# Kernel optimization log

Hardware: AMD Instinct MI355X
Metric: run time of the kernel (lower is better)

The kernel has to match this reference:

```python
import jax, jax.numpy as jnp
import numpy as np

N = 50000   # nodes
E = 800000  # edges
D = 256     # num_features == embedding_num
L = 3       # gcn layers
G = 512     # graphs in batch


def setup_inputs() -> dict:
    key = jax.random.key(0)
    ks = jax.random.split(key, 7)
    x = jax.random.normal(ks[0], (N, D), dtype=jnp.float32)
    edge_index = jax.random.randint(ks[1], (2, E), 0, N, dtype=jnp.int32)
    batch = jnp.sort(jax.random.randint(ks[2], (N,), 0, G, dtype=jnp.int32))
    s = 0.05
    Ws1 = jax.random.normal(ks[3], (L, D, D), dtype=jnp.float32) * s
    bs1 = jnp.zeros((L, D), dtype=jnp.float32)
    Ws2 = jax.random.normal(ks[4], (L, D, D), dtype=jnp.float32) * s
    bs2 = jnp.zeros((L, D), dtype=jnp.float32)
    return {"x": x, "edge_index": edge_index, "batch": batch,
            "Ws1": Ws1, "bs1": bs1, "Ws2": Ws2, "bs2": bs2}


def reference(x, edge_index, batch, Ws1, bs1, Ws2, bs2):
    src, dst = edge_index[0], edge_index[1]
    h = x
    xs = []
    for i in range(L):
        # GINConv (eps=0): h_i' = MLP( h_i + sum_{j->i} h_j )
        agg = h + jax.ops.segment_sum(h[src], dst, num_segments=N)  # [N, D]
        t = jnp.maximum(agg @ Ws1[i] + bs1[i], 0.0)                 # inner ReLU
        h = jnp.maximum(t @ Ws2[i] + bs2[i], 0.0)                   # outer F.relu
        xs.append(h)
    # global mean pool per layer output, keyed by graph id
    ones = jnp.ones((N, 1), dtype=x.dtype)
    counts = jnp.clip(jax.ops.segment_sum(ones, batch, num_segments=G), 1.0)  # [G,1]
    pooled = [jax.ops.segment_sum(h_i, batch, num_segments=G) / counts for h_i in xs]
    graph_embed = jnp.concatenate(pooled, axis=1)  # [G, L*D]
    node_embed = jnp.concatenate(xs, axis=1)       # [N, L*D]
    return graph_embed, node_embed
```

## Files before the change

kernel.cpp:

```cpp
#include <hip/hip_runtime.h>

#define NN 50000
#define EE 800000
#define DD 256
#define LL 3
#define GG 512
#define MPAD 50048

typedef __attribute__((ext_vector_type(4))) _Float16 half4;
typedef __attribute__((ext_vector_type(8))) _Float16 half8;
typedef __attribute__((ext_vector_type(16))) float floatx16;

__global__ void k_convert(const float* __restrict__ x, _Float16* __restrict__ h16) {
    int i = blockIdx.x * 256 + threadIdx.x;
    if (i >= NN * DD / 4) return;
    float4 v = ((const float4*)x)[i];
    half4 o;
    o.x = (_Float16)v.x; o.y = (_Float16)v.y; o.z = (_Float16)v.z; o.w = (_Float16)v.w;
    ((half4*)h16)[i] = o;
}

__global__ void k_hist(const int* __restrict__ dst, int* __restrict__ deg, int e) {
    int i = blockIdx.x * blockDim.x + threadIdx.x;
    if (i < e) atomicAdd(&deg[dst[i]], 1);
}

__global__ void k_scan1(const int* __restrict__ deg, int* __restrict__ rp,
                        int* __restrict__ bsum, int n) {
    __shared__ int s[1024];
    int t = threadIdx.x;
    int i = blockIdx.x * 1024 + t;
    int v = (i < n) ? deg[i] : 0;
    s[t] = v;
    __syncthreads();
    for (int off = 1; off < 1024; off <<= 1) {
        int tmp = (t >= off) ? s[t - off] : 0;
        __syncthreads();
        s[t] += tmp;
        __syncthreads();
    }
    if (i < n) rp[i] = s[t] - v;
    if (t == 1023) bsum[blockIdx.x] = s[1023];
}

__global__ void k_scan2(int* __restrict__ bsum, int nb, int* __restrict__ total_out) {
    int lane = threadIdx.x & 63;
    int v = (lane < nb) ? bsum[lane] : 0;
    int orig = v;
    for (int off = 1; off < 64; off <<= 1) {
        int u = __shfl_up(v, off);
        if (lane >= off) v += u;
    }
    if (lane < nb) bsum[lane] = v - orig;
    if (lane == 63) *total_out = v;
}

__global__ void k_scan3(int* __restrict__ rp, const int* __restrict__ bsum,
                        int* __restrict__ cursor, int n) {
    int i = blockIdx.x * 1024 + threadIdx.x;
    if (i < n) {
        int v = rp[i] + bsum[blockIdx.x];
        rp[i] = v;
        cursor[i] = v;
    }
}

__global__ void k_scatter(const int* __restrict__ src, const int* __restrict__ dst,
                          int* __restrict__ cursor, int* __restrict__ csr_src, int e) {
    int i = blockIdx.x * blockDim.x + threadIdx.x;
    if (i < e) {
        int d = dst[i];
        int pos = atomicAdd(&cursor[d], 1);
        csr_src[pos] = src[i];
    }
}

__global__ void k_wpack(const float* __restrict__ Ws1, const float* __restrict__ Ws2,
                        _Float16* __restrict__ Wp) {
    int tid  = blockIdx.x * 256 + threadIdx.x;
    int lane = tid & 63;
    int nt   = (tid >> 6) & 7;
    int ks   = (tid >> 9) & 15;
    int w    = tid >> 13;
    if (w >= 6) return;
    int l = w >> 1, s = w & 1;
    const float* W = (s == 0 ? Ws1 : Ws2) + (size_t)l * DD * DD;
    int kbase = ks * 16 + (lane >> 5) * 8;
    int n     = nt * 32 + (lane & 31);
    half8 hi;
#pragma unroll
    for (int j = 0; j < 8; ++j) hi[j] = (_Float16)W[(size_t)(kbase + j) * DD + n];
    ((half8*)Wp)[(((size_t)w * 16 + ks) * 8 + nt) * 64 + lane] = hi;
}

__global__ __launch_bounds__(256) void k_gather(
        const _Float16* __restrict__ h,
        const int* __restrict__ row_ptr,
        const int* __restrict__ csr_src,
        _Float16* __restrict__ agg) {
    __shared__ int eidx[1024];
    __shared__ int rp_s[5];
    int t = threadIdx.x, lane = t & 63, w = t >> 6;
    int n0 = blockIdx.x * 4;
    if (t < 5) {
        int nn = n0 + t;
        if (nn > NN) nn = NN;
        rp_s[t] = row_ptr[nn];
    }
    __syncthreads();
    int beg0 = rp_s[0];
    int cnt  = rp_s[4] - beg0;
    for (int i = t; i < cnt && i < 1024; i += 256) eidx[i] = csr_src[beg0 + i];
    __syncthreads();

    int n = n0 + w;
    if (n >= NN) return;
    int beg = rp_s[w] - beg0, end = rp_s[w + 1] - beg0;
    const half4* hp = (const half4*)h;
    half4 acc = hp[(size_t)n * 64 + lane];

    if (cnt <= 1024) {
        int j = beg;
        for (; j + 16 <= end; j += 16) {
            half4 v[16];
#pragma unroll
            for (int u = 0; u < 16; ++u) {
                int s = eidx[j + u];
                v[u] = hp[(size_t)s * 64 + lane];
            }
#pragma unroll
            for (int u = 0; u < 16; ++u) acc += v[u];
        }
        if (j + 8 <= end) {
            half4 v[8];
#pragma unroll
            for (int u = 0; u < 8; ++u) {
                int s = eidx[j + u];
                v[u] = hp[(size_t)s * 64 + lane];
            }
#pragma unroll
            for (int u = 0; u < 8; ++u) acc += v[u];
            j += 8;
        }
        if (j + 4 <= end) {
            half4 v[4];
#pragma unroll
            for (int u = 0; u < 4; ++u) {
                int s = eidx[j + u];
                v[u] = hp[(size_t)s * 64 + lane];
            }
            acc += v[0]; acc += v[1]; acc += v[2]; acc += v[3];
            j += 4;
        }
        for (; j < end; ++j) {
            int s = eidx[j];
            acc += hp[(size_t)s * 64 + lane];
        }
    } else {
        int j = beg;
        for (; j + 4 <= end; j += 4) {
            int s0 = csr_src[beg0 + j + 0];
            int s1 = csr_src[beg0 + j + 1];
            int s2 = csr_src[beg0 + j + 2];
            int s3 = csr_src[beg0 + j + 3];
            half4 v0 = hp[(size_t)s0 * 64 + lane];
            half4 v1 = hp[(size_t)s1 * 64 + lane];
            half4 v2 = hp[(size_t)s2 * 64 + lane];
            half4 v3 = hp[(size_t)s3 * 64 + lane];
            acc += v0; acc += v1; acc += v2; acc += v3;
        }
        for (; j < end; ++j) {
            int s = csr_src[beg0 + j];
            acc += hp[(size_t)s * 64 + lane];
        }
    }
    ((half4*)(agg + (size_t)n * DD))[lane] = acc;
}

__global__ __launch_bounds__(256) void k_mlp(
        const _Float16* __restrict__ A,
        const int* __restrict__ batch,
        const _Float16* __restrict__ Wp1, const float* __restrict__ b1,
        const _Float16* __restrict__ Wp2, const float* __restrict__ b2,
        _Float16* __restrict__ Hout,
        float* __restrict__ Fout,
        float* __restrict__ Gout) {
    __shared__ _Float16 t_lds[64 * 256];
    __shared__ int batch_s[64];
    int t    = threadIdx.x;
    int lane = t & 63;
    int w    = t >> 6;
    int wm   = w >> 1, wn = w & 1;
    int r0   = blockIdx.x * 64;

    if (t < 64) {
        int r = r0 + t;
        batch_s[t] = (r < NN) ? batch[r] : 0x7fffffff;
    }

    int arow = r0 + wm * 32 + (lane & 31);
    const half8* baseA = (const half8*)(A + (size_t)arow * DD) + (lane >> 5);
    const half8* B1    = (const half8*)Wp1;

    floatx16 acc[4];
#pragma unroll
    for (int nt = 0; nt < 4; ++nt)
#pragma unroll
        for (int i = 0; i < 16; ++i) acc[nt][i] = 0.0f;

#pragma unroll 4
    for (int ks = 0; ks < 16; ++ks) {
        half8 a = baseA[ks * 2];
#pragma unroll
        for (int nt = 0; nt < 4; ++nt) {
            half8 b = B1[(size_t)(ks * 8 + wn * 4 + nt) * 64 + lane];
            acc[nt] = __builtin_amdgcn_mfma_f32_32x32x16_f16(a, b, acc[nt], 0, 0, 0);
        }
    }

#pragma unroll
    for (int nt = 0; nt < 4; ++nt) {
        int c  = wn * 128 + nt * 32 + (lane & 31);
        float bv = b1[c];
#pragma unroll
        for (int reg = 0; reg < 16; ++reg) {
            int lr = wm * 32 + (reg & 3) + 8 * (reg >> 2) + 4 * (lane >> 5);
            float v = fmaxf(acc[nt][reg] + bv, 0.0f);
            t_lds[lr * 256 + ((((c >> 3) ^ (lr & 7)) << 3) | (c & 7))] = (_Float16)v;
        }
    }
    __syncthreads();

    const half8* B2 = (const half8*)Wp2;
    int r = wm * 32 + (lane & 31);
    floatx16 acc2[4];
#pragma unroll
    for (int nt = 0; nt < 4; ++nt)
#pragma unroll
        for (int i = 0; i < 16; ++i) acc2[nt][i] = 0.0f;

#pragma unroll 4
    for (int ks = 0; ks < 16; ++ks) {
        int kblk = ks * 2 + (lane >> 5);
        half8 a = *(const half8*)&t_lds[r * 256 + ((kblk ^ (r & 7)) << 3)];
#pragma unroll
        for (int nt = 0; nt < 4; ++nt) {
            half8 b = B2[(size_t)(ks * 8 + wn * 4 + nt) * 64 + lane];
            acc2[nt] = __builtin_amdgcn_mfma_f32_32x32x16_f16(a, b, acc2[nt], 0, 0, 0);
        }
    }

    const int rbase = wm * 32 + 4 * (lane >> 5);
#pragma unroll
    for (int nt = 0; nt < 4; ++nt) {
        int col = wn * 128 + nt * 32 + (lane & 31);
        float bv = b2[col];
#pragma unroll
        for (int reg = 0; reg < 16; ++reg) {
            int rowid = rbase + (reg & 3) + 8 * (reg >> 2);
            int row = r0 + rowid;
            if (row < NN) {
                float v = fmaxf(acc2[nt][reg] + bv, 0.0f);
                Hout[(size_t)row * DD + col] = (_Float16)v;
                Fout[(size_t)row * 768 + col] = v;
            }
        }
    }

    int lastid = NN - 1 - r0 - wm * 32;
    if (lastid >= 0) {
        if (lastid > 31) lastid = 31;
        int g0 = batch_s[wm * 32];
        int g1 = batch_s[wm * 32 + lastid];
        for (int g = g0; g <= g1; ++g) {
#pragma unroll
            for (int nt = 0; nt < 4; ++nt) {
                int col = wn * 128 + nt * 32 + (lane & 31);
                float bv = b2[col];
                float s = 0.0f;
#pragma unroll
                for (int reg = 0; reg < 16; ++reg) {
                    int rowid = rbase + (reg & 3) + 8 * (reg >> 2);
                    if (batch_s[rowid] == g)
                        s += fmaxf(acc2[nt][reg] + bv, 0.0f);
                }
                s += __shfl_xor(s, 32);
                if (lane < 32)
                    atomicAdd(&Gout[(size_t)g * 768 + col], s);
            }
        }
    }
}

__global__ void k_pool_final(const float* __restrict__ gsum,
                             const int* __restrict__ batch,
                             float* __restrict__ graph_embed) {
    int g = blockIdx.x;
    int t = threadIdx.x;
    int start, end;
    { int l = 0, h = NN; while (l < h) { int m = (l + h) >> 1; if (batch[m] < g) l = m + 1; else h = m; } start = l; }
    { int l = 0, h = NN; while (l < h) { int m = (l + h) >> 1; if (batch[m] < g + 1) l = m + 1; else h = m; } end = l; }
    int cnt = end - start;
    float inv = 1.0f / (float)(cnt > 0 ? cnt : 1);
    float4 v = ((const float4*)(gsum + (size_t)g * 768))[t];
    float4 o; o.x = v.x * inv; o.y = v.y * inv; o.z = v.z * inv; o.w = v.w * inv;
    ((float4*)(graph_embed + (size_t)g * 768))[t] = o;
}

extern "C" void kernel_launch(void* const* d_in, const int* in_sizes, int n_in,
                              void* d_out, int out_size, void* d_ws, size_t ws_size,
                              hipStream_t stream) {
    const float* x     = (const float*)d_in[0];
    const int*   ei    = (const int*)d_in[1];
    const int*   batch = (const int*)d_in[2];
    const float* Ws1   = (const float*)d_in[3];
    const float* bs1   = (const float*)d_in[4];
    const float* Ws2   = (const float*)d_in[5];
    const float* bs2   = (const float*)d_in[6];

    float* out         = (float*)d_out;
    float* graph_embed = out;
    float* node_embed  = out + (size_t)GG * 768;

    _Float16* h16   = (_Float16*)d_ws;
    _Float16* agg16 = h16 + (size_t)MPAD * DD;
    _Float16* Wp    = agg16 + (size_t)MPAD * DD;
    float* gsum     = (float*)(Wp + (size_t)6 * 65536);
    int* cursor     = (int*)(gsum + (size_t)GG * 768);
    int* bsum       = cursor + NN;
    int* csr_src    = bsum + 64;
    int* row_ptr    = csr_src + EE;

    const int* src = ei;
    const int* dst = ei + EE;

    const int NB = (NN + 1023) / 1024;

    k_convert<<<(NN * DD / 4 + 255) / 256, 256, 0, stream>>>(x, h16);
    k_wpack<<<192, 256, 0, stream>>>(Ws1, Ws2, Wp);

    hipMemsetAsync(gsum, 0, (size_t)GG * 768 * 4 + (size_t)NN * 4 + 64 * 4, stream);

    k_hist<<<(EE + 255) / 256, 256, 0, stream>>>(dst, cursor, EE);
    k_scan1<<<NB, 1024, 0, stream>>>(cursor, row_ptr, bsum, NN);
    k_scan2<<<1, 64, 0, stream>>>(bsum, NB, row_ptr + NN);
    k_scan3<<<NB, 1024, 0, stream>>>(row_ptr, bsum, cursor, NN);
    k_scatter<<<(EE + 255) / 256, 256, 0, stream>>>(src, dst, cursor, csr_src, EE);

    for (int l = 0; l < LL; ++l) {
        k_gather<<<(NN + 3) / 4, 256, 0, stream>>>(h16, row_ptr, csr_src, agg16);
        k_mlp<<<MPAD / 64, 256, 0, stream>>>(
            agg16, batch,
            Wp + (size_t)(2 * l + 0) * 65536, bs1 + (size_t)l * DD,
            Wp + (size_t)(2 * l + 1) * 65536, bs2 + (size_t)l * DD,
            h16, node_embed + (size_t)l * DD, gsum + (size_t)l * DD);
    }

    k_pool_final<<<GG, 192, 0, stream>>>(gsum, batch, graph_embed);
}
```

Before: 635.8 us.

## Fuse prep kernels, widen gather to half8 with edge split, nontemporal output

Merges the convert, weight-pack and histogram kernels into one launch selected by block index, which removes two launches. The gather now has each wave split into two halves that handle alternating edges with 16-byte half8 loads, combined by a cross-half shuffle, so more edges are in flight per wave. Node-embedding float stores become nontemporal so they do not displace the cache. The padded tail handling in the gather adds some wasted predicated work for low-degree nodes.

```diff
diff --git a/kernel.cpp b/kernel.cpp
--- a/kernel.cpp
+++ b/kernel.cpp
@@ -11,18 +11,41 @@
 typedef __attribute__((ext_vector_type(8))) _Float16 half8;
 typedef __attribute__((ext_vector_type(16))) float floatx16;
 
-__global__ void k_convert(const float* __restrict__ x, _Float16* __restrict__ h16) {
-    int i = blockIdx.x * 256 + threadIdx.x;
-    if (i >= NN * DD / 4) return;
-    float4 v = ((const float4*)x)[i];
-    half4 o;
-    o.x = (_Float16)v.x; o.y = (_Float16)v.y; o.z = (_Float16)v.z; o.w = (_Float16)v.w;
-    ((half4*)h16)[i] = o;
-}
-
-__global__ void k_hist(const int* __restrict__ dst, int* __restrict__ deg, int e) {
-    int i = blockIdx.x * blockDim.x + threadIdx.x;
-    if (i < e) atomicAdd(&deg[dst[i]], 1);
+#define CONV_B 12500
+#define WPK_B  192
+#define HIST_B 3125
+
+__global__ void k_prep(const float* __restrict__ x, _Float16* __restrict__ h16,
+                       const float* __restrict__ Ws1, const float* __restrict__ Ws2,
+                       _Float16* __restrict__ Wp,
+                       const int* __restrict__ dst, int* __restrict__ deg) {
+    int b = blockIdx.x;
+    if (b < CONV_B) {
+        int i = b * 256 + threadIdx.x;
+        if (i >= NN * DD / 4) return;
+        float4 v = ((const float4*)x)[i];
+        half4 o;
+        o.x = (_Float16)v.x; o.y = (_Float16)v.y; o.z = (_Float16)v.z; o.w = (_Float16)v.w;
+        ((half4*)h16)[i] = o;
+    } else if (b < CONV_B + WPK_B) {
+        int tid  = (b - CONV_B) * 256 + threadIdx.x;
+        int lane = tid & 63;
+        int nt   = (tid >> 6) & 7;
+        int ks   = (tid >> 9) & 15;
+        int w    = tid >> 13;
+        if (w >= 6) return;
+        int l = w >> 1, s = w & 1;
+        const float* W = (s == 0 ? Ws1 : Ws2) + (size_t)l * DD * DD;
+        int kbase = ks * 16 + (lane >> 5) * 8;
+        int n     = nt * 32 + (lane & 31);
+        half8 hi;
+#pragma unroll
+        for (int j = 0; j < 8; ++j) hi[j] = (_Float16)W[(size_t)(kbase + j) * DD + n];
+        ((half8*)Wp)[(((size_t)w * 16 + ks) * 8 + nt) * 64 + lane] = hi;
+    } else {
+        int i = (b - CONV_B - WPK_B) * 256 + threadIdx.x;
+        if (i < EE) atomicAdd(&deg[dst[i]], 1);
+    }
 }
 
 __global__ void k_scan1(const int* __restrict__ deg, int* __restrict__ rp,
@@ -75,24 +98,6 @@
     }
 }
 
-__global__ void k_wpack(const float* __restrict__ Ws1, const float* __restrict__ Ws2,
-                        _Float16* __restrict__ Wp) {
-    int tid  = blockIdx.x * 256 + threadIdx.x;
-    int lane = tid & 63;
-    int nt   = (tid >> 6) & 7;
-    int ks   = (tid >> 9) & 15;
-    int w    = tid >> 13;
-    if (w >= 6) return;
-    int l = w >> 1, s = w & 1;
-    const float* W = (s == 0 ? Ws1 : Ws2) + (size_t)l * DD * DD;
-    int kbase = ks * 16 + (lane >> 5) * 8;
-    int n     = nt * 32 + (lane & 31);
-    half8 hi;
-#pragma unroll
-    for (int j = 0; j < 8; ++j) hi[j] = (_Float16)W[(size_t)(kbase + j) * DD + n];
-    ((half8*)Wp)[(((size_t)w * 16 + ks) * 8 + nt) * 64 + lane] = hi;
-}
-
 __global__ __launch_bounds__(256) void k_gather(
         const _Float16* __restrict__ h,
         const int* __restrict__ row_ptr,
@@ -116,65 +121,71 @@
     int n = n0 + w;
     if (n >= NN) return;
     int beg = rp_s[w] - beg0, end = rp_s[w + 1] - beg0;
-    const half4* hp = (const half4*)h;
-    half4 acc = hp[(size_t)n * 64 + lane];
+    int hf = lane >> 5;
+    int cl = lane & 31;
+    const half8* hp = (const half8*)h;
+
+    half8 acc;
+#pragma unroll
+    for (int i = 0; i < 8; ++i) acc[i] = (_Float16)0;
+    if (hf == 0) acc = hp[(size_t)n * 32 + cl];
 
     if (cnt <= 1024) {
-        int j = beg;
-        for (; j + 16 <= end; j += 16) {
-            half4 v[16];
-#pragma unroll
-            for (int u = 0; u < 16; ++u) {
-                int s = eidx[j + u];
-                v[u] = hp[(size_t)s * 64 + lane];
-            }
-#pragma unroll
-            for (int u = 0; u < 16; ++u) acc += v[u];
-        }
-        if (j + 8 <= end) {
-            half4 v[8];
+        int k = beg;
+        for (; k + 16 <= end; k += 16) {
+            half8 v[8];
 #pragma unroll
             for (int u = 0; u < 8; ++u) {
-                int s = eidx[j + u];
-                v[u] = hp[(size_t)s * 64 + lane];
+                int s = eidx[k + 2 * u + hf];
+                v[u] = hp[(size_t)s * 32 + cl];
             }
 #pragma unroll
             for (int u = 0; u < 8; ++u) acc += v[u];
-            j += 8;
-        }
-        if (j + 4 <= end) {
-            half4 v[4];
-#pragma unroll
-            for (int u = 0; u < 4; ++u) {
-                int s = eidx[j + u];
-                v[u] = hp[(size_t)s * 64 + lane];
-            }
-            acc += v[0]; acc += v[1]; acc += v[2]; acc += v[3];
-            j += 4;
-        }
-        for (; j < end; ++j) {
-            int s = eidx[j];
-            acc += hp[(size_t)s * 64 + lane];
+        }
+        if (k < end) {
+#pragma unroll
+            for (int u = 0; u < 8; ++u) {
+                int e = k + 2 * u + hf;
+                half8 v;
+#pragma unroll
+                for (int i = 0; i < 8; ++i) v[i] = (_Float16)0;
+                if (e < end) v = hp[(size_t)eidx[e] * 32 + cl];
+                acc += v;
+            }
         }
     } else {
-        int j = beg;
-        for (; j + 4 <= end; j += 4) {
-            int s0 = csr_src[beg0 + j + 0];
-            int s1 = csr_src[beg0 + j + 1];
-            int s2 = csr_src[beg0 + j + 2];
-            int s3 = csr_src[beg0 + j + 3];
-            half4 v0 = hp[(size_t)s0 * 64 + lane];
-            half4 v1 = hp[(size_t)s1 * 64 + lane];
-            half4 v2 = hp[(size_t)s2 * 64 + lane];
-            half4 v3 = hp[(size_t)s3 * 64 + lane];
-            acc += v0; acc += v1; acc += v2; acc += v3;
-        }
-        for (; j < end; ++j) {
-            int s = csr_src[beg0 + j];
-            acc += hp[(size_t)s * 64 + lane];
-        }
-    }
-    ((half4*)(agg + (size_t)n * DD))[lane] = acc;
+        int k = beg;
+        for (; k + 16 <= end; k += 16) {
+            half8 v[8];
+#pragma unroll
+            for (int u = 0; u < 8; ++u) {
+                int s = csr_src[beg0 + k + 2 * u + hf];
+                v[u] = hp[(size_t)s * 32 + cl];
+            }
+#pragma unroll
+            for (int u = 0; u < 8; ++u) acc += v[u];
+        }
+        if (k < end) {
+#pragma unroll
+            for (int u = 0; u < 8; ++u) {
+                int e = k + 2 * u + hf;
+                half8 v;
+#pragma unroll
+                for (int i = 0; i < 8; ++i) v[i] = (_Float16)0;
+                if (e < end) v = hp[(size_t)csr_src[beg0 + e] * 32 + cl];
+                acc += v;
+            }
+        }
+    }
+
+    int4 ai = *(int4*)&acc;
+    int4 bi;
+    bi.x = __shfl_xor(ai.x, 32);
+    bi.y = __shfl_xor(ai.y, 32);
+    bi.z = __shfl_xor(ai.z, 32);
+    bi.w = __shfl_xor(ai.w, 32);
+    acc += *(half8*)&bi;
+    if (hf == 0) ((half8*)(agg + (size_t)n * DD))[cl] = acc;
 }
 
 __global__ __launch_bounds__(256) void k_mlp(
@@ -262,7 +273,7 @@
             if (row < NN) {
                 float v = fmaxf(acc2[nt][reg] + bv, 0.0f);
                 Hout[(size_t)row * DD + col] = (_Float16)v;
-                Fout[(size_t)row * 768 + col] = v;
+                __builtin_nontemporal_store(v, &Fout[(size_t)row * 768 + col]);
             }
         }
     }
@@ -336,12 +347,10 @@
 
     const int NB = (NN + 1023) / 1024;
 
-    k_convert<<<(NN * DD / 4 + 255) / 256, 256, 0, stream>>>(x, h16);
-    k_wpack<<<192, 256, 0, stream>>>(Ws1, Ws2, Wp);
-
     hipMemsetAsync(gsum, 0, (size_t)GG * 768 * 4 + (size_t)NN * 4 + 64 * 4, stream);
 
-    k_hist<<<(EE + 255) / 256, 256, 0, stream>>>(dst, cursor, EE);
+    k_prep<<<CONV_B + WPK_B + HIST_B, 256, 0, stream>>>(x, h16, Ws1, Ws2, Wp, dst, cursor);
+
     k_scan1<<<NB, 1024, 0, stream>>>(cursor, row_ptr, bsum, NN);
     k_scan2<<<1, 64, 0, stream>>>(bsum, NB, row_ptr + NN);
     k_scan3<<<NB, 1024, 0, stream>>>(row_ptr, bsum, cursor, NN);
```

New measurement: 618.7 us. 1.03x faster.
